# Performance work log

Hardware: AMD Instinct MI355X
Metric: run time of the kernel (lower is better)

## Reference

```python
import jax, jax.numpy as jnp
import numpy as np
from jax import lax

TS = 0.1
TRACKLENGTH = 100
CA3SIGMA = 5.0
BS, STIMUNUM, ECNUM = 256, 2, 1024
CA1NUM = 1024
CA3NUM = 1024
ACTNUM = 2


def _xavier(key, shape):
    fan_in, fan_out = shape
    std = (2.0 / (fan_in + fan_out)) ** 0.5
    return jax.random.normal(key, shape, dtype=jnp.float32) * std


def setup_inputs() -> dict:
    key = jax.random.key(0)
    ks = jax.random.split(key, 8)
    cue = jax.random.bernoulli(ks[0], 0.5, (BS, STIMUNUM, ECNUM))
    ec3_last = jax.random.uniform(ks[1], (BS, ECNUM), dtype=jnp.float32)
    ec5_last = jax.random.uniform(ks[2], (BS, ECNUM), dtype=jnp.float32)
    ca1_last = jax.random.uniform(ks[3], (BS, CA1NUM), dtype=jnp.float32)
    ca1bias = jnp.zeros((CA1NUM,), dtype=jnp.float32)
    wca3ca1 = jax.random.uniform(ks[4], (CA3NUM, CA1NUM), dtype=jnp.float32) * 0.01
    wec3ca1 = _xavier(ks[5], (ECNUM, CA1NUM))
    wca1ec5 = _xavier(ks[6], (CA1NUM, ECNUM))
    wca1act = _xavier(ks[7], (CA1NUM, ACTNUM))
    actbias = jnp.zeros((ACTNUM,), dtype=jnp.float32)
    return {"cue": cue, "ec3_last": ec3_last, "ec5_last": ec5_last, "ca1_last": ca1_last,
            "ca1bias": ca1bias, "wca3ca1": wca3ca1, "wec3ca1": wec3ca1,
            "wca1ec5": wca1ec5, "wca1act": wca1act, "actbias": actbias}


def reference(cue, ec3_last, ec5_last, ca1_last, ca1bias, wca3ca1, wec3ca1, wca1ec5, wca1act, actbias):
    T = TRACKLENGTH
    steps = jnp.arange(T, dtype=jnp.float32)                      # (T,)
    ca3center = jnp.linspace(0.0, float(T), CA3NUM)               # (ca3num,)
    # CA3 place-field responses for every step, precomputed: (T, ca3num)
    ca3all = jnp.exp(-((ca3center[None, :] - steps[:, None]) ** 2) / (CA3SIGMA ** 2) / 2.0)
    ca1drive = ca3all @ wca3ca1                                   # (T, ca1num)
    # Static cue locations: 0.08 * T * (i + 2); step matches location exactly.
    cueloc = 0.08 * T * (jnp.arange(STIMUNUM, dtype=jnp.float32) + 2.0)
    matches = steps[:, None] == cueloc[None, :]                   # (T, stimunum)
    # Per-step cue update mask: (T, bs, ecnum)
    mask_all = jnp.any(matches[:, None, :, None] & cue[None, :, :, :], axis=2)

    def step(carry, xs):
        ec3, ec5, _ = carry
        drive, mask = xs
        ca1 = jax.nn.relu(drive[None, :] * (1.0 + jax.nn.sigmoid(ec3 @ wec3ca1)) - ca1bias)
        ec5 = ec5 + 10.0 * TS * (ca1 @ wca1ec5)
        ec5 = 0.69 + 0.3 * jax.nn.sigmoid(4.0 * (ec5 - 0.3))
        ec3 = ec5 * ec3
        ec3 = jnp.where(mask, 0.4 * ec3 + 0.6, ec3)
        return (ec3, ec5, ca1), (ec3[0], ec5[0], ca1[0])

    (ec3, ec5, ca1), (ec3his, ec5his, ca1his) = lax.scan(
        step, (ec3_last, ec5_last, ca1_last), (ca1drive, mask_all))
    actCell = ca1 @ wca1act + actbias
    return (actCell, ec3his, ec5his, ca1his, ec3, ec5, ca1)
```

## Files before the change

### kernel.cpp

```cpp
#include <hip/hip_runtime.h>
#include <stdint.h>

#define NSTEP 100
#define FEAT  1024
#define SPIN_CAP (1 << 16)

typedef __attribute__((ext_vector_type(8)))  short short8;
typedef __attribute__((ext_vector_type(4)))  float fx4;
typedef __attribute__((ext_vector_type(16))) float fx16;
typedef __attribute__((ext_vector_type(2)))  unsigned int u32x2;
typedef __attribute__((ext_vector_type(4)))  int i32x4;

#define OFF_EC3   0u
#define OFF_CA1   (1u << 20)
#define OFF_DRIVE (2u << 20)
#define OFF_EC3F  (OFF_DRIVE + 425984u)
#define OFF_CA1F  (OFF_EC3F + 32768u)
#define OFF_DRVF  (OFF_CA1F + 32768u)
#define OFF_GRP   (OFF_DRVF + 4096u)
#define WS_NEED   (OFF_GRP + 4096u)

#define FSTR 32

#define GSTRIDE 32768
#define PSTRIDE (8 * GSTRIDE)

#define O_ACT 0
#define O_E3H 512
#define O_E5H (512 + 102400)
#define O_CAH (512 + 204800)
#define O_E3  (512 + 307200)
#define O_E5  (O_E3 + 262144)
#define O_CA  (O_E5 + 262144)

#define LDS_W1    0
#define LDS_W2    65536
#define LDS_RED4  131072
#define LDS_DRV   147456
#define LDS_UNI   160256
#define LDS_TOTAL 160272

__device__ __forceinline__ unsigned short f2bf(float x) {
  uint32_t u = __builtin_bit_cast(uint32_t, x);
  uint32_t r = (u + 0x7FFFu + ((u >> 16) & 1u)) >> 16;
  return (unsigned short)r;
}
__device__ __forceinline__ float sigm(float x) { return 1.0f / (1.0f + __expf(-x)); }

#define VM_DRAIN() asm volatile("s_waitcnt vmcnt(0)" ::: "memory")

__device__ __forceinline__ void ex_store(void* p, u32x2 v, bool uni) {
  if (uni) asm volatile("global_store_dwordx2 %0, %1, off sc0"     :: "v"(p), "v"(v) : "memory");
  else     asm volatile("global_store_dwordx2 %0, %1, off sc0 sc1" :: "v"(p), "v"(v) : "memory");
}
__device__ __forceinline__ void llc_store_f32(float* p, float v) {
  asm volatile("global_store_dword %0, %1, off sc0 sc1" :: "v"(p), "v"(v) : "memory");
}
__device__ __forceinline__ void flag_store(int* p, int v) {
  __hip_atomic_store(p, v, __ATOMIC_RELAXED, __HIP_MEMORY_SCOPE_AGENT);
}
__device__ __forceinline__ void flag_add(int* p) {
  __hip_atomic_fetch_add(p, 1, __ATOMIC_RELAXED, __HIP_MEMORY_SCOPE_AGENT);
}
__device__ __forceinline__ int flag_peek(const int* p) {
  return __hip_atomic_load(p, __ATOMIC_RELAXED, __HIP_MEMORY_SCOPE_AGENT);
}
__device__ __forceinline__ void flag_wait(const int* p, int tgt) {
  int sp = 0;
  while (flag_peek(p) < tgt) {
    __builtin_amdgcn_s_sleep(1);
    if (++sp > SPIN_CAP) break;
  }
}

__device__ __forceinline__ u32x2 packbf4(fx4 v) {
  u32x2 r;
  r[0] = (uint32_t)f2bf(v[0]) | ((uint32_t)f2bf(v[1]) << 16);
  r[1] = (uint32_t)f2bf(v[2]) | ((uint32_t)f2bf(v[3]) << 16);
  return r;
}

template <bool UNI>
__device__ __forceinline__ void gemm_phase_pipe(const short* __restrict__ abuf,
                                                const short* __restrict__ wl,
                                                float* __restrict__ red4, int tid,
                                                const int* __restrict__ flags, int tgt) {
  const int lane = tid & 63, w = tid >> 6;
  const int m = lane & 31, h = lane >> 5;
  const short* ap = abuf + (32 * w + h) * 256 + m * 8;
  const short* bp = wl + (32 * w + h) * 256 + m * 8;
  const int* fp = flags + lane * FSTR;
  short8 A[16] = {};
  i32x4 f = {0, 0, 0, 0};
  unsigned issuedm = 0;
  int sp = 0;
  const bool poller = (lane < 8);

#define ISSUE_PAIR(p)                                                          \
  if (newly & (1u << (p))) {                                                   \
    if (UNI) {                                                                 \
      asm volatile("global_load_dwordx4 %0, %1, off sc0"                       \
                   : "=v"(A[2 * (p)]) : "v"(ap + (2 * (p)) * 512) : "memory"); \
      asm volatile("global_load_dwordx4 %0, %1, off sc0"                       \
                   : "=v"(A[2 * (p) + 1]) : "v"(ap + (2 * (p) + 1) * 512) : "memory"); \
    } else {                                                                   \
      asm volatile("global_load_dwordx4 %0, %1, off sc0 sc1"                   \
                   : "=v"(A[2 * (p)]) : "v"(ap + (2 * (p)) * 512) : "memory"); \
      asm volatile("global_load_dwordx4 %0, %1, off sc0 sc1"                   \
                   : "=v"(A[2 * (p) + 1]) : "v"(ap + (2 * (p) + 1) * 512) : "memory"); \
    }                                                                          \
  }

#pragma unroll 1
  while (true) {
    bool mine = poller && (f[0] >= tgt) && (f[1] >= tgt) &&
                (f[2] >= tgt) && (f[3] >= tgt);
    unsigned ready = (unsigned)(__ballot(mine) & 0xFFull);
    unsigned newly = ready & ~issuedm;
    if (newly) {
      ISSUE_PAIR(0) ISSUE_PAIR(1) ISSUE_PAIR(2) ISSUE_PAIR(3)
      ISSUE_PAIR(4) ISSUE_PAIR(5) ISSUE_PAIR(6) ISSUE_PAIR(7)
      issuedm |= newly;
    }
    if (issuedm == 0xFFu) break;
    if (poller)
      asm volatile("global_load_dwordx4 %0, %1, off sc0 sc1"
                   : "=v"(f) : "v"(fp) : "memory");
    __builtin_amdgcn_s_sleep(2);
    if (++sp > SPIN_CAP) break;
  }
#undef ISSUE_PAIR

  asm volatile("s_waitcnt vmcnt(0)"
               : "+v"(A[0]), "+v"(A[1]), "+v"(A[2]), "+v"(A[3]),
                 "+v"(A[4]), "+v"(A[5]), "+v"(A[6]), "+v"(A[7]),
                 "+v"(A[8]), "+v"(A[9]), "+v"(A[10]), "+v"(A[11]),
                 "+v"(A[12]), "+v"(A[13]), "+v"(A[14]), "+v"(A[15])
               :: "memory");
  fx16 acc = 0.0f;
#pragma unroll
  for (int i = 0; i < 16; ++i) {
    short8 b = *(const short8*)(bp + i * 512);
    acc = __builtin_amdgcn_mfma_f32_32x32x16_bf16(A[i], b, acc, 0, 0, 0);
  }
#pragma unroll
  for (int i = 0; i < 16; ++i)
    red4[w * 1024 + ((i & 3) + 8 * (i >> 2) + 4 * h) * 32 + m] = acc[i];
}

extern "C" __global__ void __launch_bounds__(256)
hpcrnn_kernel(const int* __restrict__ cue,
              const float* __restrict__ ec3_last,
              const float* __restrict__ ec5_last,
              const float* __restrict__ ca1bias,
              const float* __restrict__ wca3ca1,
              const float* __restrict__ wec3ca1,
              const float* __restrict__ wca1ec5,
              const float* __restrict__ wca1act,
              const float* __restrict__ actbias,
              float* __restrict__ out,
              char* __restrict__ ws)
{
  extern __shared__ __attribute__((aligned(16))) char lds[];
  short* w1l  = (short*)(lds + LDS_W1);
  short* w2l  = (short*)(lds + LDS_W2);
  float* red4 = (float*)(lds + LDS_RED4);
  float* drvl = (float*)(lds + LDS_DRV);
  int*   unil = (int*)(lds + LDS_UNI);

  const int tid = threadIdx.x;
  const int bi  = blockIdx.x & 7;
  const int nj  = blockIdx.x >> 3;
  const int R   = bi * 32, C = nj * 32;

  short* ec3buf = (short*)(ws + OFF_EC3);
  short* ca1buf = (short*)(ws + OFF_CA1);
  float* driveg = (float*)(ws + OFF_DRIVE);
  int*   ec3flag = (int*)(ws + OFF_EC3F);
  int*   ca1flag = (int*)(ws + OFF_CA1F);
  int*   drvflag = (int*)(ws + OFF_DRVF);
  int*   grpmask = (int*)(ws + OFF_GRP);
  int*   grpcnt  = (int*)(ws + OFF_GRP) + 512;
  const int fbase = bi * 32;

  if (tid == 0) {
    int xcc;
    asm volatile("s_getreg_b32 %0, hwreg(HW_REG_XCC_ID)" : "=s"(xcc));
    __hip_atomic_fetch_or(&grpmask[bi * FSTR], 1 << (xcc & 31), __ATOMIC_RELAXED, __HIP_MEMORY_SCOPE_AGENT);
    __hip_atomic_fetch_add(&grpcnt[bi * FSTR], 1, __ATOMIC_RELAXED, __HIP_MEMORY_SCOPE_AGENT);
  }

  {
    const int c = tid & 31;
    for (int k = tid >> 5; k < FEAT; k += 8) {
      const int idx = ((k >> 3) * 32 + c) * 8 + (k & 7);
      w1l[idx] = (short)f2bf(wec3ca1[k * FEAT + C + c]);
      w2l[idx] = (short)f2bf(wca1ec5[k * FEAT + C + c]);
    }
  }

  if (tid == 0) {
    flag_wait(&grpcnt[bi * FSTR], 32);
    int cnt = flag_peek(&grpcnt[bi * FSTR]);
    int mv  = __hip_atomic_load(&grpmask[bi * FSTR], __ATOMIC_RELAXED, __HIP_MEMORY_SCOPE_AGENT);
    unil[0] = (cnt >= 32 && __popc(mv) == 1) ? 1 : 0;
  }
  __syncthreads();
  const bool uni = (unil[0] != 0);

  const int r  = tid >> 3;
  const int c0 = (tid & 7) * 4;
  const int rg = R + r;
  const int cg = C + c0;
  const size_t stoff = (size_t)(((cg >> 3) * 32 + r) * 8 + (c0 & 7));
  const size_t gbase = (size_t)bi * GSTRIDE;
  const int lane = tid & 63, wv = tid >> 6;

  const fx4 biasv  = *(const fx4*)(ca1bias + cg);
  const fx4 wact01 = *(const fx4*)(wca1act + cg * 2);
  const fx4 wact23 = *(const fx4*)(wca1act + cg * 2 + 4);
  fx4 ec3v = *(const fx4*)(ec3_last + (size_t)rg * FEAT + cg);
  fx4 ec5v = *(const fx4*)(ec5_last + (size_t)rg * FEAT + cg);
  fx4 ca1v = 0.0f;

  ex_store(ec3buf + gbase + stoff, packbf4(ec3v), uni);
  VM_DRAIN();
  if (lane == 0) flag_store(&ec3flag[(fbase + nj) * FSTR + wv], 1);

  {
    float* dred = red4;
    const int g = tid >> 5, n = tid & 31;
    for (int t = bi; t < NSTEP; t += 8) {
      float part = 0.0f;
      const float tf = (float)t;
      for (int c = g * 128; c < g * 128 + 128; ++c) {
        float d = (float)c * (100.0f / 1023.0f) - tf;
        part += __expf(d * d * -0.02f) * wca3ca1[c * FEAT + C + n];
      }
      __syncthreads();
      dred[g * 32 + n] = part;
      __syncthreads();
      if (g == 0) {
        float s = 0.0f;
#pragma unroll
        for (int gg = 0; gg < 8; ++gg) s += dred[gg * 32 + n];
        llc_store_f32(driveg + t * FEAT + C + n, s);
      }
    }
    VM_DRAIN();
    __syncthreads();
    if (tid == 0) {
      flag_add(&drvflag[nj * FSTR]);
      flag_wait(&drvflag[nj * FSTR], 8);
    }
    __syncthreads();
    for (int i = tid; i < NSTEP * 32; i += 256) {
      float v;
      asm volatile("global_load_dword %0, %1, off sc0 sc1"
                   : "=v"(v) : "v"(driveg + (i >> 5) * FEAT + (i & 31) + C) : "memory");
      asm volatile("s_waitcnt vmcnt(0)" : "+v"(v) :: "memory");
      drvl[i] = v;
    }
    __syncthreads();
  }

  for (int t = 0; t < NSTEP; ++t) {
    const size_t par = (size_t)(t & 1) * PSTRIDE;
    const int tgt = t + 1;

    if (uni) gemm_phase_pipe<true >(ec3buf + par + gbase, w1l, red4, tid,
                                    ec3flag + (fbase + 8 * wv) * FSTR, tgt);
    else     gemm_phase_pipe<false>(ec3buf + par + gbase, w1l, red4, tid,
                                    ec3flag + (fbase + 8 * wv) * FSTR, tgt);
    __syncthreads();

    {
      const int e0 = 4 * tid;
      fx4 p0 = *(const fx4*)(red4 + e0);
      fx4 p1 = *(const fx4*)(red4 + 1024 + e0);
      fx4 p2 = *(const fx4*)(red4 + 2048 + e0);
      fx4 p3 = *(const fx4*)(red4 + 3072 + e0);
      const fx4 dv = *(const fx4*)(drvl + t * 32 + c0);
#pragma unroll
      for (int j = 0; j < 4; ++j) {
        float dot = (p0[j] + p1[j]) + (p2[j] + p3[j]);
        float v = dv[j] * (1.0f + sigm(dot)) - biasv[j];
        ca1v[j] = fmaxf(v, 0.0f);
      }
      ex_store(ca1buf + par + gbase + stoff, packbf4(ca1v), uni);
    }
    VM_DRAIN();
    if (lane == 0) flag_store(&ca1flag[(fbase + nj) * FSTR + wv], t + 1);
    if (rg == 0) *(fx4*)(out + O_CAH + t * FEAT + cg) = ca1v;
    __syncthreads();

    if (uni) gemm_phase_pipe<true >(ca1buf + par + gbase, w2l, red4, tid,
                                    ca1flag + (fbase + 8 * wv) * FSTR, tgt);
    else     gemm_phase_pipe<false>(ca1buf + par + gbase, w2l, red4, tid,
                                    ca1flag + (fbase + 8 * wv) * FSTR, tgt);
    __syncthreads();

    {
      const int e0 = 4 * tid;
      fx4 p0 = *(const fx4*)(red4 + e0);
      fx4 p1 = *(const fx4*)(red4 + 1024 + e0);
      fx4 p2 = *(const fx4*)(red4 + 2048 + e0);
      fx4 p3 = *(const fx4*)(red4 + 3072 + e0);
#pragma unroll
      for (int j = 0; j < 4; ++j) {
        float e5 = ec5v[j] + ((p0[j] + p1[j]) + (p2[j] + p3[j]));
        e5 = 0.69f + 0.3f * sigm(4.0f * (e5 - 0.3f));
        ec5v[j] = e5;
        ec3v[j] = e5 * ec3v[j];
      }
      if (t == 16 || t == 24) {
        const int s = (t == 24) ? 1 : 0;
        i32x4 m = *(const i32x4*)(cue + (size_t)rg * 2048 + s * 1024 + cg);
#pragma unroll
        for (int j = 0; j < 4; ++j)
          if (m[j]) ec3v[j] = 0.4f * ec3v[j] + 0.6f;
      }
      if (t < NSTEP - 1) {
        const size_t parn = (size_t)((t + 1) & 1) * PSTRIDE;
        ex_store(ec3buf + parn + gbase + stoff, packbf4(ec3v), uni);
      }
    }
    VM_DRAIN();
    if (lane == 0 && t < NSTEP - 1)
      flag_store(&ec3flag[(fbase + nj) * FSTR + wv], t + 2);
    if (rg == 0) {
      *(fx4*)(out + O_E3H + t * FEAT + cg) = ec3v;
      *(fx4*)(out + O_E5H + t * FEAT + cg) = ec5v;
    }
    __syncthreads();
  }

  float* ared = red4;
  if (tid < 64) ared[tid] = 0.0f;
  __syncthreads();
  {
    float p0 = ca1v[0] * wact01[0] + ca1v[1] * wact01[2] +
               ca1v[2] * wact23[0] + ca1v[3] * wact23[2];
    float p1 = ca1v[0] * wact01[1] + ca1v[1] * wact01[3] +
               ca1v[2] * wact23[1] + ca1v[3] * wact23[3];
    atomicAdd(&ared[r * 2 + 0], p0);
    atomicAdd(&ared[r * 2 + 1], p1);
  }
  *(fx4*)(out + O_E3 + (size_t)rg * FEAT + cg) = ec3v;
  *(fx4*)(out + O_E5 + (size_t)rg * FEAT + cg) = ec5v;
  *(fx4*)(out + O_CA + (size_t)rg * FEAT + cg) = ca1v;
  __syncthreads();
  if (tid < 64) {
    float v = ared[tid];
    if (nj == 0) v += actbias[tid & 1];
    atomicAdd(&out[O_ACT + (R + (tid >> 1)) * 2 + (tid & 1)], v);
  }
}

extern "C" void kernel_launch(void* const* d_in, const int* in_sizes, int n_in,
                              void* d_out, int out_size, void* d_ws, size_t ws_size,
                              hipStream_t stream) {
  (void)in_sizes; (void)n_in; (void)out_size;
  if (ws_size < WS_NEED) return;

  const int*   cue      = (const int*)  d_in[0];
  const float* ec3_last = (const float*)d_in[1];
  const float* ec5_last = (const float*)d_in[2];
  const float* ca1bias  = (const float*)d_in[4];
  const float* wca3ca1  = (const float*)d_in[5];
  const float* wec3ca1  = (const float*)d_in[6];
  const float* wca1ec5  = (const float*)d_in[7];
  const float* wca1act  = (const float*)d_in[8];
  const float* actbias  = (const float*)d_in[9];

  char* ws = (char*)d_ws;
  hipMemsetAsync(ws + OFF_EC3F, 0, WS_NEED - OFF_EC3F, stream);
  hipMemsetAsync(d_out, 0, 512 * sizeof(float), stream);

  hipFuncSetAttribute(reinterpret_cast<const void*>(hpcrnn_kernel),
                      hipFuncAttributeMaxDynamicSharedMemorySize, LDS_TOTAL);

  hipLaunchKernelGGL(hpcrnn_kernel, dim3(256), dim3(256), LDS_TOTAL, stream,
                     cue, ec3_last, ec5_last, ca1bias, wca3ca1, wec3ca1,
                     wca1ec5, wca1act, actbias, (float*)d_out, ws);
}
```

Baseline: 624.2 us.

## Split workgroup into compute and dedicated flag-polling warps with LDS tokens

Doubles the workgroup to 512 threads. The four added wavefronts only poll the global inter-block readiness flags and publish per-chunk readiness tokens in LDS. The four compute wavefronts now spin on cheap LDS tokens instead of issuing their own global flag loads, so polling can overlap with compute, including early prefetch polling for the next phase. The cost is more threads per CU, a more intricate barrier protocol across both roles, and a risk of deadlock or missed tokens if the phase counters fall out of step.

```diff
diff --git a/kernel.cpp b/kernel.cpp
--- a/kernel.cpp
+++ b/kernel.cpp
@@ -38,7 +38,8 @@
 #define LDS_RED4  131072
 #define LDS_DRV   147456
 #define LDS_UNI   160256
-#define LDS_TOTAL 160272
+#define LDS_TOK   160272
+#define LDS_TOTAL 160416
 
 __device__ __forceinline__ unsigned short f2bf(float x) {
   uint32_t u = __builtin_bit_cast(uint32_t, x);
@@ -48,6 +49,12 @@
 __device__ __forceinline__ float sigm(float x) { return 1.0f / (1.0f + __expf(-x)); }
 
 #define VM_DRAIN() asm volatile("s_waitcnt vmcnt(0)" ::: "memory")
+
+__device__ __forceinline__ void wg_bar() {
+  asm volatile("s_waitcnt lgkmcnt(0)" ::: "memory");
+  __builtin_amdgcn_s_barrier();
+  asm volatile("" ::: "memory");
+}
 
 __device__ __forceinline__ void ex_store(void* p, u32x2 v, bool uni) {
   if (uni) asm volatile("global_store_dwordx2 %0, %1, off sc0"     :: "v"(p), "v"(v) : "memory");
@@ -80,21 +87,48 @@
   return r;
 }
 
+__device__ __forceinline__ unsigned poller_poll(const int* __restrict__ flags,
+                                                int ftgt, volatile int* tok,
+                                                int tval, unsigned issued,
+                                                volatile int* sreq, int sval) {
+  const int lane = threadIdx.x & 63;
+  const int* fp = flags + lane * FSTR;
+  i32x4 f = {0, 0, 0, 0};
+  int sp = 0;
+  const bool pl = (lane < 8);
+#pragma unroll 1
+  while (issued != 0xFFu) {
+    if (pl)
+      asm volatile("global_load_dwordx4 %0, %1, off sc0 sc1"
+                   : "=v"(f) : "v"(fp) : "memory");
+    bool mine = pl && (f[0] >= ftgt) && (f[1] >= ftgt) &&
+                (f[2] >= ftgt) && (f[3] >= ftgt);
+    unsigned ready = (unsigned)(__ballot(mine) & 0xFFull);
+    unsigned newly = ready & ~issued;
+    if (newly) {
+      if (pl && (newly & (1u << lane))) tok[lane] = tval;
+      issued |= newly;
+    }
+    if (issued == 0xFFu) break;
+    if (sreq && *sreq >= sval) break;
+    __builtin_amdgcn_s_sleep(2);
+    if (++sp > SPIN_CAP) break;
+  }
+  return issued;
+}
+
 template <bool UNI>
-__device__ __forceinline__ void gemm_phase_pipe(const short* __restrict__ abuf,
-                                                const short* __restrict__ wl,
-                                                float* __restrict__ red4, int tid,
-                                                const int* __restrict__ flags, int tgt) {
+__device__ __forceinline__ void gemm_phase_tok(const short* __restrict__ abuf,
+                                               const short* __restrict__ wl,
+                                               float* __restrict__ red4, int tid,
+                                               volatile int* tok, int ptgt) {
   const int lane = tid & 63, w = tid >> 6;
   const int m = lane & 31, h = lane >> 5;
   const short* ap = abuf + (32 * w + h) * 256 + m * 8;
   const short* bp = wl + (32 * w + h) * 256 + m * 8;
-  const int* fp = flags + lane * FSTR;
   short8 A[16] = {};
-  i32x4 f = {0, 0, 0, 0};
   unsigned issuedm = 0;
   int sp = 0;
-  const bool poller = (lane < 8);
 
 #define ISSUE_PAIR(p)                                                          \
   if (newly & (1u << (p))) {                                                   \
@@ -113,8 +147,8 @@
 
 #pragma unroll 1
   while (true) {
-    bool mine = poller && (f[0] >= tgt) && (f[1] >= tgt) &&
-                (f[2] >= tgt) && (f[3] >= tgt);
+    int tv = (lane < 8) ? tok[lane] : 0;
+    bool mine = (lane < 8) && (tv >= ptgt);
     unsigned ready = (unsigned)(__ballot(mine) & 0xFFull);
     unsigned newly = ready & ~issuedm;
     if (newly) {
@@ -123,10 +157,7 @@
       issuedm |= newly;
     }
     if (issuedm == 0xFFu) break;
-    if (poller)
-      asm volatile("global_load_dwordx4 %0, %1, off sc0 sc1"
-                   : "=v"(f) : "v"(fp) : "memory");
-    __builtin_amdgcn_s_sleep(2);
+    __builtin_amdgcn_s_sleep(1);
     if (++sp > SPIN_CAP) break;
   }
 #undef ISSUE_PAIR
@@ -148,7 +179,7 @@
     red4[w * 1024 + ((i & 3) + 8 * (i >> 2) + 4 * h) * 32 + m] = acc[i];
 }
 
-extern "C" __global__ void __launch_bounds__(256)
+extern "C" __global__ void __launch_bounds__(512)
 hpcrnn_kernel(const int* __restrict__ cue,
               const float* __restrict__ ec3_last,
               const float* __restrict__ ec5_last,
@@ -167,6 +198,8 @@
   float* red4 = (float*)(lds + LDS_RED4);
   float* drvl = (float*)(lds + LDS_DRV);
   int*   unil = (int*)(lds + LDS_UNI);
+  volatile int* toklds = (volatile int*)(lds + LDS_TOK);
+  volatile int* sreql  = toklds + 32;
 
   const int tid = threadIdx.x;
   const int bi  = blockIdx.x & 7;
@@ -182,6 +215,9 @@
   int*   grpmask = (int*)(ws + OFF_GRP);
   int*   grpcnt  = (int*)(ws + OFF_GRP) + 512;
   const int fbase = bi * 32;
+  const int lane = tid & 63, wv = tid >> 6;
+
+  if (tid < 36) toklds[tid] = 0;
 
   if (tid == 0) {
     int xcc;
@@ -190,7 +226,7 @@
     __hip_atomic_fetch_add(&grpcnt[bi * FSTR], 1, __ATOMIC_RELAXED, __HIP_MEMORY_SCOPE_AGENT);
   }
 
-  {
+  if (tid < 256) {
     const int c = tid & 31;
     for (int k = tid >> 5; k < FEAT; k += 8) {
       const int idx = ((k >> 3) * 32 + c) * 8 + (k & 7);
@@ -214,31 +250,34 @@
   const int cg = C + c0;
   const size_t stoff = (size_t)(((cg >> 3) * 32 + r) * 8 + (c0 & 7));
   const size_t gbase = (size_t)bi * GSTRIDE;
-  const int lane = tid & 63, wv = tid >> 6;
-
-  const fx4 biasv  = *(const fx4*)(ca1bias + cg);
-  const fx4 wact01 = *(const fx4*)(wca1act + cg * 2);
-  const fx4 wact23 = *(const fx4*)(wca1act + cg * 2 + 4);
-  fx4 ec3v = *(const fx4*)(ec3_last + (size_t)rg * FEAT + cg);
-  fx4 ec5v = *(const fx4*)(ec5_last + (size_t)rg * FEAT + cg);
-  fx4 ca1v = 0.0f;
-
-  ex_store(ec3buf + gbase + stoff, packbf4(ec3v), uni);
-  VM_DRAIN();
-  if (lane == 0) flag_store(&ec3flag[(fbase + nj) * FSTR + wv], 1);
+
+  fx4 biasv = 0.0f, wact01 = 0.0f, wact23 = 0.0f;
+  fx4 ec3v = 0.0f, ec5v = 0.0f, ca1v = 0.0f;
+  if (tid < 256) {
+    biasv  = *(const fx4*)(ca1bias + cg);
+    wact01 = *(const fx4*)(wca1act + cg * 2);
+    wact23 = *(const fx4*)(wca1act + cg * 2 + 4);
+    ec3v = *(const fx4*)(ec3_last + (size_t)rg * FEAT + cg);
+    ec5v = *(const fx4*)(ec5_last + (size_t)rg * FEAT + cg);
+    ex_store(ec3buf + gbase + stoff, packbf4(ec3v), uni);
+    VM_DRAIN();
+    if (lane == 0) flag_store(&ec3flag[(fbase + nj) * FSTR + wv], 1);
+  }
 
   {
     float* dred = red4;
     const int g = tid >> 5, n = tid & 31;
     for (int t = bi; t < NSTEP; t += 8) {
       float part = 0.0f;
-      const float tf = (float)t;
-      for (int c = g * 128; c < g * 128 + 128; ++c) {
-        float d = (float)c * (100.0f / 1023.0f) - tf;
-        part += __expf(d * d * -0.02f) * wca3ca1[c * FEAT + C + n];
+      if (tid < 256) {
+        const float tf = (float)t;
+        for (int c = g * 128; c < g * 128 + 128; ++c) {
+          float d = (float)c * (100.0f / 1023.0f) - tf;
+          part += __expf(d * d * -0.02f) * wca3ca1[c * FEAT + C + n];
+        }
       }
       __syncthreads();
-      dred[g * 32 + n] = part;
+      if (tid < 256) dred[g * 32 + n] = part;
       __syncthreads();
       if (g == 0) {
         float s = 0.0f;
@@ -254,7 +293,7 @@
       flag_wait(&drvflag[nj * FSTR], 8);
     }
     __syncthreads();
-    for (int i = tid; i < NSTEP * 32; i += 256) {
+    for (int i = tid; i < NSTEP * 32; i += 512) {
       float v;
       asm volatile("global_load_dword %0, %1, off sc0 sc1"
                    : "=v"(v) : "v"(driveg + (i >> 5) * FEAT + (i & 31) + C) : "memory");
@@ -264,91 +303,113 @@
     __syncthreads();
   }
 
-  for (int t = 0; t < NSTEP; ++t) {
-    const size_t par = (size_t)(t & 1) * PSTRIDE;
-    const int tgt = t + 1;
-
-    if (uni) gemm_phase_pipe<true >(ec3buf + par + gbase, w1l, red4, tid,
-                                    ec3flag + (fbase + 8 * wv) * FSTR, tgt);
-    else     gemm_phase_pipe<false>(ec3buf + par + gbase, w1l, red4, tid,
-                                    ec3flag + (fbase + 8 * wv) * FSTR, tgt);
-    __syncthreads();
-
-    {
-      const int e0 = 4 * tid;
-      fx4 p0 = *(const fx4*)(red4 + e0);
-      fx4 p1 = *(const fx4*)(red4 + 1024 + e0);
-      fx4 p2 = *(const fx4*)(red4 + 2048 + e0);
-      fx4 p3 = *(const fx4*)(red4 + 3072 + e0);
-      const fx4 dv = *(const fx4*)(drvl + t * 32 + c0);
-#pragma unroll
-      for (int j = 0; j < 4; ++j) {
-        float dot = (p0[j] + p1[j]) + (p2[j] + p3[j]);
-        float v = dv[j] * (1.0f + sigm(dot)) - biasv[j];
-        ca1v[j] = fmaxf(v, 0.0f);
+  if (wv < 4) {
+    volatile int* tok = toklds + wv * 8;
+    for (int t = 0; t < NSTEP; ++t) {
+      const size_t par = (size_t)(t & 1) * PSTRIDE;
+
+      if (uni) gemm_phase_tok<true >(ec3buf + par + gbase, w1l, red4, tid, tok, 2 * t + 1);
+      else     gemm_phase_tok<false>(ec3buf + par + gbase, w1l, red4, tid, tok, 2 * t + 1);
+      if (lane == 0) sreql[wv] = 4 * t + 1;
+      wg_bar();
+
+      {
+        const int e0 = 4 * tid;
+        fx4 p0 = *(const fx4*)(red4 + e0);
+        fx4 p1 = *(const fx4*)(red4 + 1024 + e0);
+        fx4 p2 = *(const fx4*)(red4 + 2048 + e0);
+        fx4 p3 = *(const fx4*)(red4 + 3072 + e0);
+        const fx4 dv = *(const fx4*)(drvl + t * 32 + c0);
+#pragma unroll
+        for (int j = 0; j < 4; ++j) {
+          float dot = (p0[j] + p1[j]) + (p2[j] + p3[j]);
+          float v = dv[j] * (1.0f + sigm(dot)) - biasv[j];
+          ca1v[j] = fmaxf(v, 0.0f);
+        }
+        ex_store(ca1buf + par + gbase + stoff, packbf4(ca1v), uni);
       }
-      ex_store(ca1buf + par + gbase + stoff, packbf4(ca1v), uni);
-    }
-    VM_DRAIN();
-    if (lane == 0) flag_store(&ca1flag[(fbase + nj) * FSTR + wv], t + 1);
-    if (rg == 0) *(fx4*)(out + O_CAH + t * FEAT + cg) = ca1v;
-    __syncthreads();
-
-    if (uni) gemm_phase_pipe<true >(ca1buf + par + gbase, w2l, red4, tid,
-                                    ca1flag + (fbase + 8 * wv) * FSTR, tgt);
-    else     gemm_phase_pipe<false>(ca1buf + par + gbase, w2l, red4, tid,
-                                    ca1flag + (fbase + 8 * wv) * FSTR, tgt);
-    __syncthreads();
-
-    {
-      const int e0 = 4 * tid;
-      fx4 p0 = *(const fx4*)(red4 + e0);
-      fx4 p1 = *(const fx4*)(red4 + 1024 + e0);
-      fx4 p2 = *(const fx4*)(red4 + 2048 + e0);
-      fx4 p3 = *(const fx4*)(red4 + 3072 + e0);
-#pragma unroll
-      for (int j = 0; j < 4; ++j) {
-        float e5 = ec5v[j] + ((p0[j] + p1[j]) + (p2[j] + p3[j]));
-        e5 = 0.69f + 0.3f * sigm(4.0f * (e5 - 0.3f));
-        ec5v[j] = e5;
-        ec3v[j] = e5 * ec3v[j];
+      VM_DRAIN();
+      if (lane == 0) flag_store(&ca1flag[(fbase + nj) * FSTR + wv], t + 1);
+      if (rg == 0) *(fx4*)(out + O_CAH + t * FEAT + cg) = ca1v;
+      if (lane == 0) sreql[wv] = 4 * t + 2;
+      wg_bar();
+
+      if (uni) gemm_phase_tok<true >(ca1buf + par + gbase, w2l, red4, tid, tok, 2 * t + 2);
+      else     gemm_phase_tok<false>(ca1buf + par + gbase, w2l, red4, tid, tok, 2 * t + 2);
+      if (lane == 0) sreql[wv] = 4 * t + 3;
+      wg_bar();
+
+      {
+        const int e0 = 4 * tid;
+        fx4 p0 = *(const fx4*)(red4 + e0);
+        fx4 p1 = *(const fx4*)(red4 + 1024 + e0);
+        fx4 p2 = *(const fx4*)(red4 + 2048 + e0);
+        fx4 p3 = *(const fx4*)(red4 + 3072 + e0);
+#pragma unroll
+        for (int j = 0; j < 4; ++j) {
+          float e5 = ec5v[j] + ((p0[j] + p1[j]) + (p2[j] + p3[j]));
+          e5 = 0.69f + 0.3f * sigm(4.0f * (e5 - 0.3f));
+          ec5v[j] = e5;
+          ec3v[j] = e5 * ec3v[j];
+        }
+        if (t == 16 || t == 24) {
+          const int s = (t == 24) ? 1 : 0;
+          i32x4 mq = *(const i32x4*)(cue + (size_t)rg * 2048 + s * 1024 + cg);
+#pragma unroll
+          for (int j = 0; j < 4; ++j)
+            if (mq[j]) ec3v[j] = 0.4f * ec3v[j] + 0.6f;
+        }
+        if (t < NSTEP - 1) {
+          const size_t parn = (size_t)((t + 1) & 1) * PSTRIDE;
+          ex_store(ec3buf + parn + gbase + stoff, packbf4(ec3v), uni);
+        }
       }
-      if (t == 16 || t == 24) {
-        const int s = (t == 24) ? 1 : 0;
-        i32x4 m = *(const i32x4*)(cue + (size_t)rg * 2048 + s * 1024 + cg);
-#pragma unroll
-        for (int j = 0; j < 4; ++j)
-          if (m[j]) ec3v[j] = 0.4f * ec3v[j] + 0.6f;
+      VM_DRAIN();
+      if (lane == 0 && t < NSTEP - 1)
+        flag_store(&ec3flag[(fbase + nj) * FSTR + wv], t + 2);
+      if (rg == 0) {
+        *(fx4*)(out + O_E3H + t * FEAT + cg) = ec3v;
+        *(fx4*)(out + O_E5H + t * FEAT + cg) = ec5v;
       }
-      if (t < NSTEP - 1) {
-        const size_t parn = (size_t)((t + 1) & 1) * PSTRIDE;
-        ex_store(ec3buf + parn + gbase + stoff, packbf4(ec3v), uni);
-      }
-    }
-    VM_DRAIN();
-    if (lane == 0 && t < NSTEP - 1)
-      flag_store(&ec3flag[(fbase + nj) * FSTR + wv], t + 2);
-    if (rg == 0) {
-      *(fx4*)(out + O_E3H + t * FEAT + cg) = ec3v;
-      *(fx4*)(out + O_E5H + t * FEAT + cg) = ec5v;
-    }
-    __syncthreads();
+      if (lane == 0) sreql[wv] = 4 * t + 4;
+      wg_bar();
+    }
+  } else {
+    const int cwv = wv - 4;
+    const int* f1 = ec3flag + (fbase + 8 * cwv) * FSTR;
+    const int* f2 = ca1flag + (fbase + 8 * cwv) * FSTR;
+    volatile int* tok = toklds + cwv * 8;
+    volatile int* srq = sreql + cwv;
+    unsigned carry1 = 0;
+    for (int t = 0; t < NSTEP; ++t) {
+      carry1 = poller_poll(f1, t + 1, tok, 2 * t + 1, carry1, nullptr, 0);
+      wg_bar();
+      unsigned iss2 = poller_poll(f2, t + 1, tok, 2 * t + 2, 0u, srq, 4 * t + 2);
+      wg_bar();
+      iss2 = poller_poll(f2, t + 1, tok, 2 * t + 2, iss2, nullptr, 0);
+      wg_bar();
+      unsigned c1n = 0;
+      if (t < NSTEP - 1)
+        c1n = poller_poll(f1, t + 2, tok, 2 * t + 3, 0u, srq, 4 * t + 4);
+      wg_bar();
+      carry1 = c1n;
+    }
   }
 
   float* ared = red4;
   if (tid < 64) ared[tid] = 0.0f;
   __syncthreads();
-  {
+  if (tid < 256) {
     float p0 = ca1v[0] * wact01[0] + ca1v[1] * wact01[2] +
                ca1v[2] * wact23[0] + ca1v[3] * wact23[2];
     float p1 = ca1v[0] * wact01[1] + ca1v[1] * wact01[3] +
                ca1v[2] * wact23[1] + ca1v[3] * wact23[3];
     atomicAdd(&ared[r * 2 + 0], p0);
     atomicAdd(&ared[r * 2 + 1], p1);
-  }
-  *(fx4*)(out + O_E3 + (size_t)rg * FEAT + cg) = ec3v;
-  *(fx4*)(out + O_E5 + (size_t)rg * FEAT + cg) = ec5v;
-  *(fx4*)(out + O_CA + (size_t)rg * FEAT + cg) = ca1v;
+    *(fx4*)(out + O_E3 + (size_t)rg * FEAT + cg) = ec3v;
+    *(fx4*)(out + O_E5 + (size_t)rg * FEAT + cg) = ec5v;
+    *(fx4*)(out + O_CA + (size_t)rg * FEAT + cg) = ca1v;
+  }
   __syncthreads();
   if (tid < 64) {
     float v = ared[tid];
@@ -380,7 +441,7 @@
   hipFuncSetAttribute(reinterpret_cast<const void*>(hpcrnn_kernel),
                       hipFuncAttributeMaxDynamicSharedMemorySize, LDS_TOTAL);
 
-  hipLaunchKernelGGL(hpcrnn_kernel, dim3(256), dim3(256), LDS_TOTAL, stream,
+  hipLaunchKernelGGL(hpcrnn_kernel, dim3(256), dim3(512), LDS_TOTAL, stream,
                      cue, ec3_last, ec5_last, ca1bias, wca3ca1, wec3ca1,
                      wca1ec5, wca1act, actbias, (float*)d_out, ws);
 }
```

After: 1.035 ms. 65.8% more time.
